# Kernel tuning notes

Hardware: AMD Instinct MI355X
Metric: run time of the kernel (lower is better)

The kernel has to match this reference:

```python
import jax, jax.numpy as jnp
import numpy as np

MAX_DISP = 4  # max_displacement
PAD = MAX_DISP
ODIM = 2 * MAX_DISP + 1  # 9 -> 81 cost-volume channels


def setup_inputs() -> dict:
    key = jax.random.key(0)
    k1, k2 = jax.random.split(key)
    B, C, H, W = 4, 256, 96, 192
    x1 = jax.random.normal(k1, (B, C, H, W), dtype=jnp.float32)
    x2 = jax.random.normal(k2, (B, C, H, W), dtype=jnp.float32)
    return {"x1": x1, "x2": x2}


def reference(x1, x2):
    B, C, H, W = x1.shape
    # zero-pad x2 spatially by PAD on each side (matches F.pad([pad]*4))
    x2p = jnp.pad(x2, ((0, 0), (0, 0), (PAD, PAD), (PAD, PAD)))
    cv = []
    for i in range(ODIM):          # fixed 9x9 displacement grid
        for j in range(ODIM):
            shifted = jax.lax.dynamic_slice(
                x2p, (0, 0, i, j), (B, C, H, W))
            # mean over channel dim -> [B, H, W]
            cv.append(jnp.mean(x1 * shifted, axis=1))
    return jnp.stack(cv, axis=1)  # [B, 81, H, W]
```

## Files before the change

kernel.cpp:

```cpp
#include <hip/hip_runtime.h>
#include <stddef.h>


#define NB 4
#define NC 256
#define HH 96
#define WW 192
#define TW 16
#define TH 8
#define KC 32
#define NROWS 16

#define KS 264
#define RS 1096
#define XBI(row, kg, n) ((row) * RS + (kg) * KS + (n) * 8)

typedef __attribute__((ext_vector_type(8))) short bf16x8;
typedef __attribute__((ext_vector_type(4))) float f32x4;

__device__ __forceinline__ unsigned short f2bf(float f) {
    union { float f; unsigned u; } c; c.f = f;
    unsigned r = c.u + 0x7FFFu + ((c.u >> 16) & 1u);
    return (unsigned short)(r >> 16);
}

__global__ __launch_bounds__(512, 2) void corr_mfma(
    const float* __restrict__ x1, const float* __restrict__ x2,
    float* __restrict__ out)
{
    __shared__ union {
        unsigned short xb[NROWS * RS];
        float band[TH][9][9][18];
    } lds;

    const int tid  = threadIdx.x;
    const int wv   = tid >> 6;
    const int lane = tid & 63;
    const int col  = lane & 15;
    const int q    = lane >> 4;
    const int w0   = blockIdx.x * TW;
    const int h0   = blockIdx.y * TH;
    const int b    = blockIdx.z;
    const int h    = h0 + wv;

    f32x4 acc[9][2];
#pragma unroll
    for (int di = 0; di < 9; ++di) {
        acc[di][0] = (f32x4)0.0f;
        acc[di][1] = (f32x4)0.0f;
    }

    for (int kc = 0; kc < NC; kc += KC) {
        if (kc) __syncthreads();

#pragma unroll
        for (int t0 = 0; t0 < 2; ++t0) {
            int t = tid + t0 * 512;
            if (t < 768) {
                int seg = t % 6;
                int row = (t / 6) & 15;
                int cg  = t / 96;
                int gh  = h0 - 4 + row;
                int gw  = w0 - 4 + seg * 4;
                bool ok = (gh >= 0) & (gh < HH) & (gw >= 0) & (gw + 3 < WW);
                float vv[4][4];
#pragma unroll
                for (int i = 0; i < 4; ++i) {
                    float4 ld = make_float4(0.f, 0.f, 0.f, 0.f);
                    if (ok) {
                        size_t idx = ((size_t)((b * NC + kc + cg * 4 + i) * HH + gh)) * WW + gw;
                        ld = *(const float4*)&x2[idx];
                    }
                    vv[i][0] = ld.x; vv[i][1] = ld.y; vv[i][2] = ld.z; vv[i][3] = ld.w;
                }
                int kg = cg >> 1;
                int k0 = 4 * (cg & 1);
#pragma unroll
                for (int p = 0; p < 4; ++p) {
                    ushort4 pk;
                    pk.x = f2bf(vv[0][p]); pk.y = f2bf(vv[1][p]);
                    pk.z = f2bf(vv[2][p]); pk.w = f2bf(vv[3][p]);
                    *(ushort4*)&lds.xb[XBI(row, kg, seg * 4 + p) + k0] = pk;
                }
            }
        }
        __syncthreads();

        bf16x8 a;
#pragma unroll
        for (int j = 0; j < 8; ++j) {
            size_t idx = ((size_t)((b * NC + kc + q * 8 + j) * HH + h)) * WW + w0 + col;
            a[j] = (short)f2bf(x1[idx]);
        }

#pragma unroll
        for (int di = 0; di < 9; ++di) {
            int r = wv + di;
            bf16x8 b0 = *(const bf16x8*)&lds.xb[XBI(r, q, col)];
            bf16x8 b1 = *(const bf16x8*)&lds.xb[XBI(r, q, col + 16)];
            acc[di][0] = __builtin_amdgcn_mfma_f32_16x16x32_bf16(a, b0, acc[di][0], 0, 0, 0);
            acc[di][1] = __builtin_amdgcn_mfma_f32_16x16x32_bf16(a, b1, acc[di][1], 0, 0, 0);
        }
    }

    __syncthreads();

#pragma unroll
    for (int di = 0; di < 9; ++di)
#pragma unroll
        for (int half = 0; half < 2; ++half)
#pragma unroll
            for (int r = 0; r < 4; ++r) {
                int m  = q * 4 + r;
                int dj = half * 16 + col - m;
                if (dj >= 0 && dj < 9)
                    lds.band[wv][di][dj][m] = acc[di][half][r];
            }
    __syncthreads();

    const float scale = 1.0f / 256.0f;
#pragma unroll
    for (int it = 0; it < 21; ++it) {
        int combo = it * 4 + q;
        if (combo < 81) {
            float v = lds.band[wv][combo / 9][combo % 9][col];
            out[((size_t)((b * 81 + combo) * HH + h)) * WW + w0 + col] = v * scale;
        }
    }
}

extern "C" void kernel_launch(void* const* d_in, const int* in_sizes, int n_in,
                              void* d_out, int out_size, void* d_ws, size_t ws_size,
                              hipStream_t stream) {
    const float* x1 = (const float*)d_in[0];
    const float* x2 = (const float*)d_in[1];
    float* out = (float*)d_out;

    dim3 grid(WW / TW, HH / TH, NB);
    corr_mfma<<<grid, 512, 0, stream>>>(x1, x2, out);
}
```

Before: 261.1 us.

## Prefetch next channel chunk into registers to overlap global loads with MFMA

Global loads of x2 and x1 for the next 32-channel chunk are issued into registers before the current chunk's MFMAs, then converted and stored to LDS at the start of the next iteration. This software pipelining hides global memory latency behind compute. The load mapping changes from 4-channel groups to 2-channel pairs across 3 passes, and launch bounds drop to 1 block per SM to make room for the extra prefetch registers, which may reduce occupancy.

```diff
diff --git a/kernel.cpp b/kernel.cpp
--- a/kernel.cpp
+++ b/kernel.cpp
@@ -24,7 +24,7 @@
     return (unsigned short)(r >> 16);
 }
 
-__global__ __launch_bounds__(512, 2) void corr_mfma(
+__global__ __launch_bounds__(512, 1) void corr_mfma(
     const float* __restrict__ x1, const float* __restrict__ x2,
     float* __restrict__ out)
 {
@@ -50,47 +50,72 @@
         acc[di][1] = (f32x4)0.0f;
     }
 
-    for (int kc = 0; kc < NC; kc += KC) {
-        if (kc) __syncthreads();
+    float pf[24];
+    float pa[8];
 
+#define STAGE_LOAD(kc_)                                                        \
+    {                                                                          \
+        const int kcv = (kc_);                                                 \
+        _Pragma("unroll")                                                      \
+        for (int k = 0; k < 3; ++k) {                                          \
+            int t   = tid + k * 512;                                           \
+            int seg = t % 6;                                                   \
+            int row = (t / 6) & 15;                                            \
+            int cp  = t / 96;                                                  \
+            int gh  = h0 - 4 + row;                                            \
+            int gw  = w0 - 4 + seg * 4;                                        \
+            bool ok = (gh >= 0) & (gh < HH) & (gw >= 0) & (gw <= WW - 4);      \
+            _Pragma("unroll")                                                  \
+            for (int e = 0; e < 2; ++e) {                                      \
+                float4 ld = make_float4(0.f, 0.f, 0.f, 0.f);                   \
+                if (ok) {                                                      \
+                    size_t idx = ((size_t)((b * NC + kcv + cp * 2 + e) * HH + gh)) * WW + gw; \
+                    ld = *(const float4*)&x2[idx];                             \
+                }                                                              \
+                *(float4*)&pf[(k * 2 + e) * 4] = ld;                           \
+            }                                                                  \
+        }                                                                      \
+    }
+
+#define X1_LOAD(kc_)                                                           \
+    {                                                                          \
+        const int kcv = (kc_);                                                 \
+        _Pragma("unroll")                                                      \
+        for (int j = 0; j < 8; ++j) {                                          \
+            size_t idx = ((size_t)((b * NC + kcv + q * 8 + j) * HH + h)) * WW + w0 + col; \
+            pa[j] = x1[idx];                                                   \
+        }                                                                      \
+    }
+
+    STAGE_LOAD(0);
+    X1_LOAD(0);
+
+    for (int ci = 0; ci < 8; ++ci) {
 #pragma unroll
-        for (int t0 = 0; t0 < 2; ++t0) {
-            int t = tid + t0 * 512;
-            if (t < 768) {
-                int seg = t % 6;
-                int row = (t / 6) & 15;
-                int cg  = t / 96;
-                int gh  = h0 - 4 + row;
-                int gw  = w0 - 4 + seg * 4;
-                bool ok = (gh >= 0) & (gh < HH) & (gw >= 0) & (gw + 3 < WW);
-                float vv[4][4];
+        for (int k = 0; k < 3; ++k) {
+            int t   = tid + k * 512;
+            int seg = t % 6;
+            int row = (t / 6) & 15;
+            int cp  = t / 96;
+            int kg  = cp >> 2;
+            int k0  = (cp & 3) * 2;
 #pragma unroll
-                for (int i = 0; i < 4; ++i) {
-                    float4 ld = make_float4(0.f, 0.f, 0.f, 0.f);
-                    if (ok) {
-                        size_t idx = ((size_t)((b * NC + kc + cg * 4 + i) * HH + gh)) * WW + gw;
-                        ld = *(const float4*)&x2[idx];
-                    }
-                    vv[i][0] = ld.x; vv[i][1] = ld.y; vv[i][2] = ld.z; vv[i][3] = ld.w;
-                }
-                int kg = cg >> 1;
-                int k0 = 4 * (cg & 1);
-#pragma unroll
-                for (int p = 0; p < 4; ++p) {
-                    ushort4 pk;
-                    pk.x = f2bf(vv[0][p]); pk.y = f2bf(vv[1][p]);
-                    pk.z = f2bf(vv[2][p]); pk.w = f2bf(vv[3][p]);
-                    *(ushort4*)&lds.xb[XBI(row, kg, seg * 4 + p) + k0] = pk;
-                }
+            for (int p = 0; p < 4; ++p) {
+                ushort2 v;
+                v.x = f2bf(pf[(k * 2 + 0) * 4 + p]);
+                v.y = f2bf(pf[(k * 2 + 1) * 4 + p]);
+                *(ushort2*)&lds.xb[XBI(row, kg, seg * 4 + p) + k0] = v;
             }
         }
         __syncthreads();
 
         bf16x8 a;
 #pragma unroll
-        for (int j = 0; j < 8; ++j) {
-            size_t idx = ((size_t)((b * NC + kc + q * 8 + j) * HH + h)) * WW + w0 + col;
-            a[j] = (short)f2bf(x1[idx]);
+        for (int j = 0; j < 8; ++j) a[j] = (short)f2bf(pa[j]);
+
+        if (ci < 7) {
+            STAGE_LOAD((ci + 1) * KC);
+            X1_LOAD((ci + 1) * KC);
         }
 
 #pragma unroll
@@ -101,9 +126,8 @@
             acc[di][0] = __builtin_amdgcn_mfma_f32_16x16x32_bf16(a, b0, acc[di][0], 0, 0, 0);
             acc[di][1] = __builtin_amdgcn_mfma_f32_16x16x32_bf16(a, b1, acc[di][1], 0, 0, 0);
         }
+        __syncthreads();
     }
-
-    __syncthreads();
 
 #pragma unroll
     for (int di = 0; di < 9; ++di)
```

After: 245.3 us. -6.0%, faster.

## Double-buffer LDS staging with register prefetch, new LDS layout and block swizzle

Applied to the files above, without the earlier changes.

Turns the channel loop into a software pipeline: the global loads of x2 and x1 for the next 32-channel chunk are issued into registers before the MFMA loop runs on the current LDS buffer, with two LDS buffers so only one barrier is needed per iteration. The LDS layout changes to 4-channel groups loaded as float2 pairs, and the bf16 packing uses the hardware pack intrinsic. The grid becomes 1D with an XCD-aware block remap, and launch bounds rise to 4 blocks per CU. The risks are higher register pressure and a larger LDS footprint that may cap occupancy, plus changed global coalescing.

```diff
diff --git a/kernel.cpp b/kernel.cpp
--- a/kernel.cpp
+++ b/kernel.cpp
@@ -1,4 +1,5 @@
 #include <hip/hip_runtime.h>
+#include <hip/hip_bf16.h>
 #include <stddef.h>
 
 
@@ -6,30 +7,35 @@
 #define NC 256
 #define HH 96
 #define WW 192
+#define CHW (HH * WW)
 #define TW 16
 #define TH 8
 #define KC 32
 #define NROWS 16
-
-#define KS 264
-#define RS 1096
-#define XBI(row, kg, n) ((row) * RS + (kg) * KS + (n) * 8)
+#define KS4 100
+#define RS4 808
+#define BUFSH (NROWS * RS4)
 
 typedef __attribute__((ext_vector_type(8))) short bf16x8;
 typedef __attribute__((ext_vector_type(4))) float f32x4;
 
-__device__ __forceinline__ unsigned short f2bf(float f) {
-    union { float f; unsigned u; } c; c.f = f;
-    unsigned r = c.u + 0x7FFFu + ((c.u >> 16) & 1u);
-    return (unsigned short)(r >> 16);
+union Frag { unsigned long long u[2]; unsigned int w[4]; bf16x8 v; };
+
+__device__ __forceinline__ unsigned int pk2(float a, float b) {
+    __hip_bfloat162 t = __float22bfloat162_rn(make_float2(a, b));
+    union { __hip_bfloat162 h; unsigned int u; } c; c.h = t; return c.u;
 }
 
-__global__ __launch_bounds__(512, 2) void corr_mfma(
+__device__ __forceinline__ void lds_barrier() {
+    __asm__ volatile("s_waitcnt lgkmcnt(0)\n\ts_barrier" ::: "memory");
+}
+
+__global__ __launch_bounds__(512, 4) void corr_mfma(
     const float* __restrict__ x1, const float* __restrict__ x2,
     float* __restrict__ out)
 {
     __shared__ union {
-        unsigned short xb[NROWS * RS];
+        unsigned short xb[2][BUFSH];
         float band[TH][9][9][18];
     } lds;
 
@@ -38,10 +44,27 @@
     const int lane = tid & 63;
     const int col  = lane & 15;
     const int q    = lane >> 4;
-    const int w0   = blockIdx.x * TW;
-    const int h0   = blockIdx.y * TH;
-    const int b    = blockIdx.z;
-    const int h    = h0 + wv;
+
+    const int nid = (blockIdx.x & 7) * 72 + (blockIdx.x >> 3);
+    const int w0  = (nid % 12) * TW;
+    const int h0  = ((nid / 12) % 12) * TH;
+    const int b   = nid / 144;
+    const int h   = h0 + wv;
+
+    int  toff[3]; int tlds[3]; bool tok[3];
+#pragma unroll
+    for (int k = 0; k < 3; ++k) {
+        int t   = tid + k * 512;
+        int w2  = t % 12;
+        int row = (t / 12) & 15;
+        int cg  = t / 192;
+        int gh  = h0 - 4 + row;
+        int gw  = w0 - 4 + w2 * 2;
+        tok[k]  = (gh >= 0) & (gh < HH) & (gw >= 0) & (gw < WW - 1);
+        toff[k] = ((b * NC + cg * 4) * HH + gh) * WW + gw;
+        tlds[k] = row * RS4 + cg * KS4 + w2 * 8;
+    }
+    const int x1off = ((b * NC + q * 8) * HH + h) * WW + w0 + col;
 
     f32x4 acc[9][2];
 #pragma unroll
@@ -50,56 +73,58 @@
         acc[di][1] = (f32x4)0.0f;
     }
 
-    for (int kc = 0; kc < NC; kc += KC) {
-        if (kc) __syncthreads();
+    float pf[3][4][2];
+    float pa[8];
+
+#define STAGE_LOAD(KCV)                                                        \
+    _Pragma("unroll")                                                          \
+    for (int k = 0; k < 3; ++k) {                                              \
+        int o = toff[k] + (KCV) * CHW;                                         \
+        _Pragma("unroll")                                                      \
+        for (int i = 0; i < 4; ++i) {                                          \
+            float2 v = make_float2(0.f, 0.f);                                  \
+            if (tok[k]) v = *(const float2*)&x2[o + i * CHW];                  \
+            pf[k][i][0] = v.x; pf[k][i][1] = v.y;                              \
+        }                                                                      \
+    }
+
+#define X1_LOAD(KCV)                                                           \
+    _Pragma("unroll")                                                          \
+    for (int j = 0; j < 8; ++j) pa[j] = x1[x1off + ((KCV) + j) * CHW];
+
+    STAGE_LOAD(0)
+    X1_LOAD(0)
+
+    for (int ci = 0; ci < 8; ++ci) {
+        unsigned short* xb = lds.xb[ci & 1];
 
 #pragma unroll
-        for (int t0 = 0; t0 < 2; ++t0) {
-            int t = tid + t0 * 512;
-            if (t < 768) {
-                int seg = t % 6;
-                int row = (t / 6) & 15;
-                int cg  = t / 96;
-                int gh  = h0 - 4 + row;
-                int gw  = w0 - 4 + seg * 4;
-                bool ok = (gh >= 0) & (gh < HH) & (gw >= 0) & (gw + 3 < WW);
-                float vv[4][4];
+        for (int k = 0; k < 3; ++k) {
 #pragma unroll
-                for (int i = 0; i < 4; ++i) {
-                    float4 ld = make_float4(0.f, 0.f, 0.f, 0.f);
-                    if (ok) {
-                        size_t idx = ((size_t)((b * NC + kc + cg * 4 + i) * HH + gh)) * WW + gw;
-                        ld = *(const float4*)&x2[idx];
-                    }
-                    vv[i][0] = ld.x; vv[i][1] = ld.y; vv[i][2] = ld.z; vv[i][3] = ld.w;
-                }
-                int kg = cg >> 1;
-                int k0 = 4 * (cg & 1);
-#pragma unroll
-                for (int p = 0; p < 4; ++p) {
-                    ushort4 pk;
-                    pk.x = f2bf(vv[0][p]); pk.y = f2bf(vv[1][p]);
-                    pk.z = f2bf(vv[2][p]); pk.w = f2bf(vv[3][p]);
-                    *(ushort4*)&lds.xb[XBI(row, kg, seg * 4 + p) + k0] = pk;
-                }
+            for (int p = 0; p < 2; ++p) {
+                uint2 u = make_uint2(pk2(pf[k][0][p], pf[k][1][p]),
+                                     pk2(pf[k][2][p], pf[k][3][p]));
+                *(uint2*)&xb[tlds[k] + p * 4] = u;
             }
         }
-        __syncthreads();
+        Frag fa;
+#pragma unroll
+        for (int jj = 0; jj < 4; ++jj) fa.w[jj] = pk2(pa[2 * jj], pa[2 * jj + 1]);
 
-        bf16x8 a;
-#pragma unroll
-        for (int j = 0; j < 8; ++j) {
-            size_t idx = ((size_t)((b * NC + kc + q * 8 + j) * HH + h)) * WW + w0 + col;
-            a[j] = (short)f2bf(x1[idx]);
-        }
+        if (ci < 7) { STAGE_LOAD((ci + 1) * KC) X1_LOAD((ci + 1) * KC) }
+
+        lds_barrier();
 
 #pragma unroll
         for (int di = 0; di < 9; ++di) {
-            int r = wv + di;
-            bf16x8 b0 = *(const bf16x8*)&lds.xb[XBI(r, q, col)];
-            bf16x8 b1 = *(const bf16x8*)&lds.xb[XBI(r, q, col + 16)];
-            acc[di][0] = __builtin_amdgcn_mfma_f32_16x16x32_bf16(a, b0, acc[di][0], 0, 0, 0);
-            acc[di][1] = __builtin_amdgcn_mfma_f32_16x16x32_bf16(a, b1, acc[di][1], 0, 0, 0);
+            int rb = (wv + di) * RS4 + q * (2 * KS4) + col * 4;
+            Frag b0, b1;
+            b0.u[0] = *(const unsigned long long*)&xb[rb];
+            b0.u[1] = *(const unsigned long long*)&xb[rb + KS4];
+            b1.u[0] = *(const unsigned long long*)&xb[rb + 64];
+            b1.u[1] = *(const unsigned long long*)&xb[rb + KS4 + 64];
+            acc[di][0] = __builtin_amdgcn_mfma_f32_16x16x32_bf16(fa.v, b0.v, acc[di][0], 0, 0, 0);
+            acc[di][1] = __builtin_amdgcn_mfma_f32_16x16x32_bf16(fa.v, b1.v, acc[di][1], 0, 0, 0);
         }
     }
 
@@ -136,6 +161,5 @@
     const float* x2 = (const float*)d_in[1];
     float* out = (float*)d_out;
 
-    dim3 grid(WW / TW, HH / TH, NB);
-    corr_mfma<<<grid, 512, 0, stream>>>(x1, x2, out);
+    corr_mfma<<<dim3(576), dim3(512), 0, stream>>>(x1, x2, out);
 }
```

Result: no change. 261.9 us (+0.3%).

## Load MFMA operands directly from global with register double-buffering, drop LDS staging

Applied to the files above, without the earlier changes.

Replaces the shared-memory staging of x2 with per-wave direct global loads into registers, double-buffered across displacement rows and channel chunks so loads for the next step overlap the current MFMAs. The block shrinks to 4 waves (TH=4) with higher occupancy bounds, and the block-wide barriers are removed since each wave reads only its own band slice in LDS. The aim is to cut LDS traffic and barrier stalls. In exchange, each wave re-reads overlapping x2 rows from global and cache, about 9x redundant, and register pressure goes up.

```diff
diff --git a/kernel.cpp b/kernel.cpp
--- a/kernel.cpp
+++ b/kernel.cpp
@@ -1,4 +1,5 @@
 #include <hip/hip_runtime.h>
+#include <hip/hip_bf16.h>
 #include <stddef.h>
 
 
@@ -6,32 +7,26 @@
 #define NC 256
 #define HH 96
 #define WW 192
+#define CHW (HH * WW)
 #define TW 16
-#define TH 8
+#define TH 4
 #define KC 32
-#define NROWS 16
-
-#define KS 264
-#define RS 1096
-#define XBI(row, kg, n) ((row) * RS + (kg) * KS + (n) * 8)
 
 typedef __attribute__((ext_vector_type(8))) short bf16x8;
 typedef __attribute__((ext_vector_type(4))) float f32x4;
 
-__device__ __forceinline__ unsigned short f2bf(float f) {
-    union { float f; unsigned u; } c; c.f = f;
-    unsigned r = c.u + 0x7FFFu + ((c.u >> 16) & 1u);
-    return (unsigned short)(r >> 16);
+union Frag { unsigned long long u[2]; unsigned int w[4]; bf16x8 v; };
+
+__device__ __forceinline__ unsigned int pk2(float a, float b) {
+    __hip_bfloat162 t = __float22bfloat162_rn(make_float2(a, b));
+    union { __hip_bfloat162 h; unsigned int u; } c; c.h = t; return c.u;
 }
 
-__global__ __launch_bounds__(512, 2) void corr_mfma(
+__global__ __launch_bounds__(256, 3) void corr_direct(
     const float* __restrict__ x1, const float* __restrict__ x2,
     float* __restrict__ out)
 {
-    __shared__ union {
-        unsigned short xb[NROWS * RS];
-        float band[TH][9][9][18];
-    } lds;
+    __shared__ float band[TH][9][9][18];
 
     const int tid  = threadIdx.x;
     const int wv   = tid >> 6;
@@ -43,6 +38,23 @@
     const int b    = blockIdx.z;
     const int h    = h0 + wv;
 
+    const float* x1b = x1 + (size_t)b * NC * CHW;
+    const float* x2b = x2 + (size_t)b * NC * CHW;
+
+    const int ac0  = w0 - 4 + col;
+    const int ac1  = ac0 + 16;
+    const bool okw0 = (ac0 >= 0) & (ac0 < WW);
+    const bool okw1 = (ac1 >= 0) & (ac1 < WW);
+    const int cl0 = ac0 < 0 ? 0 : (ac0 > WW - 1 ? WW - 1 : ac0);
+    const int cl1 = ac1 < 0 ? 0 : (ac1 > WW - 1 ? WW - 1 : ac1);
+    int voffB0[8], voffB1[8];
+#pragma unroll
+    for (int j = 0; j < 8; ++j) {
+        voffB0[j] = (q * 8 + j) * CHW + cl0;
+        voffB1[j] = (q * 8 + j) * CHW + cl1;
+    }
+    const int voffA = (q * 8) * CHW + col;
+
     f32x4 acc[9][2];
 #pragma unroll
     for (int di = 0; di < 9; ++di) {
@@ -50,60 +62,84 @@
         acc[di][1] = (f32x4)0.0f;
     }
 
-    for (int kc = 0; kc < NC; kc += KC) {
-        if (kc) __syncthreads();
+    float pb[2][16];
+    float pa0[8], pa1[8];
 
+#define ISSUE_B(KCH_, DI_, DST)                                                \
+    {                                                                          \
+        int row_ = h + (DI_) - 4;                                              \
+        row_ = row_ < 0 ? 0 : (row_ > HH - 1 ? HH - 1 : row_);                 \
+        int sb_ = __builtin_amdgcn_readfirstlane((KCH_) * CHW + row_ * WW);    \
+        const float* p_ = x2b + sb_;                                           \
+        _Pragma("unroll")                                                      \
+        for (int j_ = 0; j_ < 8; ++j_) (DST)[j_] = p_[voffB0[j_]];             \
+        _Pragma("unroll")                                                      \
+        for (int j_ = 0; j_ < 8; ++j_) (DST)[8 + j_] = p_[voffB1[j_]];         \
+    }
+
+#define ISSUE_A(KCH_, DST)                                                     \
+    {                                                                          \
+        int sb_ = __builtin_amdgcn_readfirstlane((KCH_) * CHW + h * WW + w0);  \
+        const float* p_ = x1b + sb_;                                           \
+        _Pragma("unroll")                                                      \
+        for (int j_ = 0; j_ < 8; ++j_) (DST)[j_] = p_[voffA + j_ * CHW];       \
+    }
+
+#define PROC(DI_, PB_, FA_)                                                    \
+    {                                                                          \
+        int row_ = h + (DI_) - 4;                                              \
+        if ((unsigned)row_ < (unsigned)HH) {                                   \
+            Frag b0_, b1_;                                                     \
+            _Pragma("unroll")                                                  \
+            for (int jj_ = 0; jj_ < 4; ++jj_) {                                \
+                float u0_ = okw0 ? (PB_)[2 * jj_]     : 0.0f;                  \
+                float u1_ = okw0 ? (PB_)[2 * jj_ + 1] : 0.0f;                  \
+                b0_.w[jj_] = pk2(u0_, u1_);                                    \
+                float v0_ = okw1 ? (PB_)[8 + 2 * jj_]     : 0.0f;              \
+                float v1_ = okw1 ? (PB_)[8 + 2 * jj_ + 1] : 0.0f;              \
+                b1_.w[jj_] = pk2(v0_, v1_);                                    \
+            }                                                                  \
+            acc[DI_][0] = __builtin_amdgcn_mfma_f32_16x16x32_bf16(             \
+                (FA_).v, b0_.v, acc[DI_][0], 0, 0, 0);                         \
+            acc[DI_][1] = __builtin_amdgcn_mfma_f32_16x16x32_bf16(             \
+                (FA_).v, b1_.v, acc[DI_][1], 0, 0, 0);                         \
+        }                                                                      \
+    }
+
+    ISSUE_A(0, pa0)
+    ISSUE_B(0, 0, pb[0])
+
+    Frag fa;
+#pragma unroll 1
+    for (int cc = 0; cc < 4; ++cc) {
+        const int c0 = cc * 2;
 #pragma unroll
-        for (int t0 = 0; t0 < 2; ++t0) {
-            int t = tid + t0 * 512;
-            if (t < 768) {
-                int seg = t % 6;
-                int row = (t / 6) & 15;
-                int cg  = t / 96;
-                int gh  = h0 - 4 + row;
-                int gw  = w0 - 4 + seg * 4;
-                bool ok = (gh >= 0) & (gh < HH) & (gw >= 0) & (gw + 3 < WW);
-                float vv[4][4];
+        for (int t = 0; t < 18; ++t) {
+            const int lc  = t / 9;
+            const int di  = t % 9;
+            const int par = t & 1;
+
+            if (di == 0) {
+                const float* pav = (lc == 0) ? pa0 : pa1;
 #pragma unroll
-                for (int i = 0; i < 4; ++i) {
-                    float4 ld = make_float4(0.f, 0.f, 0.f, 0.f);
-                    if (ok) {
-                        size_t idx = ((size_t)((b * NC + kc + cg * 4 + i) * HH + gh)) * WW + gw;
-                        ld = *(const float4*)&x2[idx];
-                    }
-                    vv[i][0] = ld.x; vv[i][1] = ld.y; vv[i][2] = ld.z; vv[i][3] = ld.w;
-                }
-                int kg = cg >> 1;
-                int k0 = 4 * (cg & 1);
-#pragma unroll
-                for (int p = 0; p < 4; ++p) {
-                    ushort4 pk;
-                    pk.x = f2bf(vv[0][p]); pk.y = f2bf(vv[1][p]);
-                    pk.z = f2bf(vv[2][p]); pk.w = f2bf(vv[3][p]);
-                    *(ushort4*)&lds.xb[XBI(row, kg, seg * 4 + p) + k0] = pk;
-                }
+                for (int jj = 0; jj < 4; ++jj)
+                    fa.w[jj] = pk2(pav[2 * jj], pav[2 * jj + 1]);
             }
-        }
-        __syncthreads();
 
-        bf16x8 a;
-#pragma unroll
-        for (int j = 0; j < 8; ++j) {
-            size_t idx = ((size_t)((b * NC + kc + q * 8 + j) * HH + h)) * WW + w0 + col;
-            a[j] = (short)f2bf(x1[idx]);
-        }
+            {
+                const int tn = t + 1, lcn = tn / 9, din = tn % 9;
+                int kn = c0 + lcn; if (kn > 7) kn = 7;
+                ISSUE_B(kn * KC, din, pb[1 - par])
+            }
+            if (di == 4) {
+                int an = c0 + lc + 1; if (an > 7) an = 7;
+                if (lc == 0) { ISSUE_A(an * KC, pa1) }
+                else         { ISSUE_A(an * KC, pa0) }
+            }
 
-#pragma unroll
-        for (int di = 0; di < 9; ++di) {
-            int r = wv + di;
-            bf16x8 b0 = *(const bf16x8*)&lds.xb[XBI(r, q, col)];
-            bf16x8 b1 = *(const bf16x8*)&lds.xb[XBI(r, q, col + 16)];
-            acc[di][0] = __builtin_amdgcn_mfma_f32_16x16x32_bf16(a, b0, acc[di][0], 0, 0, 0);
-            acc[di][1] = __builtin_amdgcn_mfma_f32_16x16x32_bf16(a, b1, acc[di][1], 0, 0, 0);
+            PROC(di, pb[par], fa)
         }
     }
-
-    __syncthreads();
 
 #pragma unroll
     for (int di = 0; di < 9; ++di)
@@ -114,16 +150,15 @@
                 int m  = q * 4 + r;
                 int dj = half * 16 + col - m;
                 if (dj >= 0 && dj < 9)
-                    lds.band[wv][di][dj][m] = acc[di][half][r];
+                    band[wv][di][dj][m] = acc[di][half][r];
             }
-    __syncthreads();
 
     const float scale = 1.0f / 256.0f;
 #pragma unroll
     for (int it = 0; it < 21; ++it) {
         int combo = it * 4 + q;
         if (combo < 81) {
-            float v = lds.band[wv][combo / 9][combo % 9][col];
+            float v = band[wv][combo / 9][combo % 9][col];
             out[((size_t)((b * 81 + combo) * HH + h)) * WW + w0 + col] = v * scale;
         }
     }
@@ -137,5 +172,5 @@
     float* out = (float*)d_out;
 
     dim3 grid(WW / TW, HH / TH, NB);
-    corr_mfma<<<grid, 512, 0, stream>>>(x1, x2, out);
+    corr_direct<<<grid, 256, 0, stream>>>(x1, x2, out);
 }
```

New measurement: 340.6 us. 1.3x slower.
